# Performance work log

Hardware: AMD Instinct MI355X
Metric: run time of the kernel (lower is better)

## Reference

```python
import jax, jax.numpy as jnp
import numpy as np

DX = 8e-6      # pixel pitch (m)
Z = 0.05       # propagation distance (m)
B, C, H, W = 8, 3, 1024, 1024


def setup_inputs() -> dict:
    key = jax.random.key(0)
    k1, k2 = jax.random.split(key)
    x_real = jax.random.normal(k1, (B, C, H, W), dtype=jnp.float32)
    x_imag = jax.random.normal(k2, (B, C, H, W), dtype=jnp.float32)
    wavelengths = jnp.asarray([450e-9, 532e-9, 632.8e-9], dtype=jnp.float32)
    return {"x_real": x_real, "x_imag": x_imag, "wavelengths": wavelengths}


def _transfer_function(wavelengths, h, w, dx, z):
    # Angular-spectrum transfer function per wavelength: [C, H, W] complex64
    fx = jnp.fft.fftfreq(w, d=dx).astype(jnp.float32)  # [W]
    fy = jnp.fft.fftfreq(h, d=dx).astype(jnp.float32)  # [H]
    f2 = fy[:, None] ** 2 + fx[None, :] ** 2           # [H, W]
    lam = wavelengths[:, None, None]                   # [C, 1, 1]
    arg = 1.0 - (lam ** 2) * f2[None]                  # [C, H, W]
    kz = (2.0 * jnp.pi / lam) * z * jnp.sqrt(jnp.maximum(arg, 0.0))
    Hc = jnp.exp(1j * kz.astype(jnp.complex64))
    # zero out evanescent components
    return jnp.where(arg > 0.0, Hc, jnp.zeros((), dtype=jnp.complex64))


def reference(x_real, x_imag, wavelengths):
    # Batched angular-spectrum propagation, one wavelength per channel.
    x = (x_real + 1j * x_imag).astype(jnp.complex64)   # [B, C, H, W]
    Hc = _transfer_function(wavelengths, H, W, DX, Z)  # [C, H, W]
    Xf = jnp.fft.fft2(x, axes=(-2, -1))
    out = jnp.fft.ifft2(Xf * Hc[None], axes=(-2, -1))  # [B, C, H, W] complex
    # return real/imag stacked so output is a float tensor: [2, B, C, H, W]
    return jnp.stack([out.real.astype(jnp.float32), out.imag.astype(jnp.float32)], axis=0)
```

## Files before the change

kernel.cpp:

```cpp
#include <hip/hip_runtime.h>
#include <math.h>


#define NIMG 24

__device__ __forceinline__ float2 cadd(float2 a, float2 b){ return make_float2(a.x+b.x, a.y+b.y); }
__device__ __forceinline__ float2 csub(float2 a, float2 b){ return make_float2(a.x-b.x, a.y-b.y); }
__device__ __forceinline__ float2 cmul(float2 a, float c, float s){ return make_float2(a.x*c - a.y*s, a.x*s + a.y*c); }

__device__ __forceinline__ int SW(int j) {
    int b = j << 3;
    return b ^ (((b >> 7) & 7) << 4);
}

__device__ __forceinline__ float2 computeH(float lam, int ky, int kx) {
    int iy = (ky < 512) ? ky : ky - 1024;
    int ix = (kx < 512) ? kx : kx - 1024;
    const double recip = 1.0 / (1024.0 * 8e-06);
    float fy = (float)((double)iy * recip);
    float fx = (float)((double)ix * recip);
    float f2  = __fadd_rn(__fmul_rn(fy, fy), __fmul_rn(fx, fx));
    float l2  = __fmul_rn(lam, lam);
    float arg = __fsub_rn(1.0f, __fmul_rn(l2, f2));
    float2 h = make_float2(0.0f, 0.0f);
    if (arg > 0.0f) {
        float t  = __fdiv_rn(6.28318530717958647692f, lam);
        t        = __fmul_rn(t, 0.05f);
        float kz = __fmul_rn(t, __fsqrt_rn(arg));
        double s, c;
        sincos((double)kz, &s, &c);
        const float sc = 9.5367431640625e-07f;
        h = make_float2((float)c * sc, (float)s * sc);
    }
    return h;
}

__global__ __launch_bounds__(256) void build_H_T(float2* __restrict__ Htab,
                                                 const float* __restrict__ wl) {
    int idx = blockIdx.x * 256 + threadIdx.x;
    int c   = idx >> 20;
    int rem = idx & 1048575;
    Htab[idx] = computeH(wl[c], rem & 1023, rem >> 10);
}

template<int SIGN>
__device__ __forceinline__ void dft4nt(float2& a0, float2& a1, float2& a2, float2& a3) {
    float2 t0 = cadd(a0, a2), t1 = csub(a0, a2);
    float2 t2 = cadd(a1, a3), t3 = csub(a1, a3);
    a0 = cadd(t0, t2);
    a2 = csub(t0, t2);
    a1 = make_float2(t1.x - SIGN * t3.y, t1.y + SIGN * t3.x);
    a3 = make_float2(t1.x + SIGN * t3.y, t1.y - SIGN * t3.x);
}
template<int SIGN>
__device__ __forceinline__ void dft4(float2& a0, float2& a1, float2& a2, float2& a3,
                                     float c1, float s1) {
    float c2 = c1*c1 - s1*s1, s2 = 2.f*c1*s1;
    float c3 = c2*c1 - s2*s1, s3 = s2*c1 + c2*s1;
    a1 = cmul(a1, c1, s1);
    a2 = cmul(a2, c2, s2);
    a3 = cmul(a3, c3, s3);
    dft4nt<SIGN>(a0, a1, a2, a3);
}

#define WSYNC() do { asm volatile("s_waitcnt lgkmcnt(0)" ::: "memory"); \
                     __builtin_amdgcn_wave_barrier(); } while (0)


__device__ __forceinline__ void ldsToRegs(char* cb, int l, float2 (&v)[4][4]) {
    const int swzE = (((l >> 4)    ) & 7) << 4;
    const int swzO = (((l >> 4) + 4) & 7) << 4;
    char* rbE = cb + ((8 * l) ^ swzE);
    char* rbO = cb + ((8 * l) ^ swzO);
    #pragma unroll
    for (int k = 0; k < 4; ++k) {
        #pragma unroll
        for (int r = 0; r < 4; ++r) {
            const int tt = k + 4 * r;
            v[k][r] = *(const float2*)(((tt & 1) ? rbO : rbE) + 512 * tt);
        }
    }
}

template<int SIGN>
__device__ __forceinline__ void fftA(char* cb, int l, float2 (&v)[4][4]) {
    const float SPI8 = SIGN * 0.39269908169872415481f;
    #pragma unroll
    for (int k = 0; k < 4; ++k) dft4nt<SIGN>(v[k][0], v[k][1], v[k][2], v[k][3]);
    dft4nt<SIGN>(v[0][0], v[1][0], v[2][0], v[3][0]);
    #pragma unroll
    for (int q = 1; q < 4; ++q) {
        float s1, c1; __sincosf((float)q * SPI8, &s1, &c1);
        dft4<SIGN>(v[0][q], v[1][q], v[2][q], v[3][q], c1, s1);
    }
    char* wb = cb + 128 * l;
    const int L7 = l & 7;
    #pragma unroll
    for (int p = 0; p < 4; ++p) {
        *(float4*)(wb + 16 * ((2*p+0) ^ L7)) =
            make_float4(v[p][0].x, v[p][0].y, v[p][1].x, v[p][1].y);
        *(float4*)(wb + 16 * ((2*p+1) ^ L7)) =
            make_float4(v[p][2].x, v[p][2].y, v[p][3].x, v[p][3].y);
    }
}

template<int SIGN>
__device__ __forceinline__ void fftB(char* cb, int l) {
    const float SPI32  = SIGN * 0.09817477042468103870f;
    const float SPI128 = SIGN * 0.02454369260617025967f;
    const int swzE = (((l >> 4)    ) & 7) << 4;
    const int swzO = (((l >> 4) + 4) & 7) << 4;
    char* rbE = cb + ((8 * l) ^ swzE);
    char* rbO = cb + ((8 * l) ^ swzO);
    float2 v[4][4];
    #pragma unroll
    for (int k = 0; k < 4; ++k) {
        #pragma unroll
        for (int r = 0; r < 4; ++r) {
            const int tt = k + 4 * r;
            v[k][r] = *(const float2*)(((tt & 1) ? rbO : rbE) + 512 * tt);
        }
    }
    const int jm2 = l & 15;
    float s1, c1; __sincosf((float)jm2 * SPI32, &s1, &c1);
    #pragma unroll
    for (int k = 0; k < 4; ++k) dft4<SIGN>(v[k][0], v[k][1], v[k][2], v[k][3], c1, s1);
    const int lo8 = 8 * (l & 15);
    const int hi  = 2048 * (l >> 4);
    #pragma unroll
    for (int q = 0; q < 4; ++q) {
        float s1b, c1b; __sincosf((float)(jm2 + 16 * q) * SPI128, &s1b, &c1b);
        dft4<SIGN>(v[0][q], v[1][q], v[2][q], v[3][q], c1b, s1b);
        #pragma unroll
        for (int p = 0; p < 4; ++p) {
            const int K = ((q + 4 * p) & 7) << 4;
            *(float2*)(cb + (lo8 ^ K) + hi + 128 * q + 512 * p) = v[p][q];
        }
    }
}

template<int SIGN>
__device__ __forceinline__ void fftC(int l, float2 (&v)[4][4]) {
    const float SPI512 = SIGN * 0.00613592315154256492f;
    #pragma unroll
    for (int m = 0; m < 4; ++m) {
        float s1, c1; __sincosf((float)(l + 64 * m) * SPI512, &s1, &c1);
        dft4<SIGN>(v[m][0], v[m][1], v[m][2], v[m][3], c1, s1);
    }
}

__global__ __launch_bounds__(1024) void k1_rows_T16(const float* __restrict__ xr,
                                                    const float* __restrict__ xi,
                                                    float2* __restrict__ T) {
    extern __shared__ char lds[];
    const int t = threadIdx.x, w = t >> 6, l = t & 63;
    const int img = blockIdx.x >> 6;
    const int b0  = blockIdx.x & 63;
    const int y0  = b0 << 4;
    const long long ib = (long long)img << 20;
    char* cb = lds + 8192 * w;

    const float* rr = xr + ib + (long long)(y0 + w) * 1024;
    const float* ri = xi + ib + (long long)(y0 + w) * 1024;
    float2 v[4][4];
    #pragma unroll
    for (int k = 0; k < 4; ++k) {
        #pragma unroll
        for (int r = 0; r < 4; ++r) {
            const int p = l + 64 * (k + 4 * r);
            v[k][r] = make_float2(rr[p], ri[p]);
        }
    }
    fftA<-1>(cb, l, v); WSYNC();
    fftB<-1>(cb, l);    WSYNC();
    ldsToRegs(cb, l, v);
    fftC<-1>(l, v);
    __syncthreads();

    {
        const int w8 = w << 3;
        #pragma unroll
        for (int m = 0; m < 4; ++m) {
            #pragma unroll
            for (int q = 0; q < 4; ++q) {
                const int p  = l + 64 * (m + 4 * q);
                const int sx = (((p >> 1) & 7) << 4) | (((p >> 4) & 1) << 3);
                *(float2*)(lds + p * 128 + (w8 ^ sx)) = v[m][q];
            }
        }
    }
    __syncthreads();

    {
        const int j = l >> 3;
        const int xbase = (w << 3) + (l & 7);
        const bool sw = (w >> 1) & 1;
        #pragma unroll
        for (int i = 0; i < 8; ++i) {
            const int x   = xbase + (i << 7);
            const int s70 = ((x >> 1) & 7) << 4;
            float4 g = *(const float4*)(lds + x * 128 + ((16 * j) ^ s70));
            if (sw) g = make_float4(g.z, g.w, g.x, g.y);
            const int rb = (b0 + x) & 63;
            *(float4*)(T + ib + (long long)x * 1024 + (rb << 4) + 2 * j) = g;
        }
    }
}

__global__ __launch_bounds__(256, 4) void k2_cols_H(float2* __restrict__ T,
                                                    const float2* __restrict__ Htab,
                                                    const float* __restrict__ wl) {
    __shared__ float4 ldsb[2048];
    char* lds = (char*)ldsb;
    const int t = threadIdx.x, w = t >> 6, l = t & 63;
    const int img = blockIdx.x >> 8;
    const int x   = ((blockIdx.x & 255) << 2) + w;
    const int lamIdx = img % 3;
    char* cb = lds + 8192 * w;
    float2* col = T + ((long long)img << 20) + (long long)x * 1024;

    const int xl15 = l & 15, lhi = l >> 4;
    #define CIDX(tt) (((((lhi) + 4 * (tt) + x) & 63) << 4) + xl15)

    float2 v[4][4];
    #pragma unroll
    for (int k = 0; k < 4; ++k) {
        #pragma unroll
        for (int r = 0; r < 4; ++r)
            v[k][r] = col[CIDX(k + 4 * r)];
    }
    fftA<-1>(cb, l, v); WSYNC();
    fftB<-1>(cb, l);    WSYNC();

    float2 h[4][4];
    if (Htab) {
        const float2* hrow = Htab + ((long long)lamIdx << 20) + (long long)x * 1024;
        #pragma unroll
        for (int m = 0; m < 4; ++m) {
            #pragma unroll
            for (int q = 0; q < 4; ++q)
                h[m][q] = hrow[l + 64 * (m + 4 * q)];
        }
    } else {
        const float lam = wl[lamIdx];
        #pragma unroll
        for (int m = 0; m < 4; ++m) {
            #pragma unroll
            for (int q = 0; q < 4; ++q)
                h[m][q] = computeH(lam, l + 64 * (m + 4 * q), x);
        }
    }

    ldsToRegs(cb, l, v);
    fftC<-1>(l, v);

    #pragma unroll
    for (int m = 0; m < 4; ++m) {
        #pragma unroll
        for (int q = 0; q < 4; ++q) {
            float2 a = v[m][q], hh = h[m][q];
            v[m][q] = make_float2(a.x * hh.x - a.y * hh.y, a.x * hh.y + a.y * hh.x);
        }
    }
    WSYNC();

    fftA<1>(cb, l, v); WSYNC();
    fftB<1>(cb, l);    WSYNC();
    ldsToRegs(cb, l, v);
    fftC<1>(l, v);

    #pragma unroll
    for (int m = 0; m < 4; ++m) {
        #pragma unroll
        for (int q = 0; q < 4; ++q)
            col[CIDX(m + 4 * q)] = v[m][q];
    }
    #undef CIDX
}

__global__ __launch_bounds__(1024) void k3_irows_T16(const float2* __restrict__ T,
                                                     float* __restrict__ outr,
                                                     float* __restrict__ outi) {
    extern __shared__ char lds[];
    const int t = threadIdx.x, w = t >> 6, l = t & 63;
    const int img = blockIdx.x >> 6;
    const int b0  = blockIdx.x & 63;
    const int y0  = b0 << 4;
    const long long ib = (long long)img << 20;

    {
        const int rb = (b0 + t) & 63;
        const float4* src = (const float4*)(T + ib + (long long)t * 1024 + (rb << 4));
        const int sx = SW(t);
        #pragma unroll
        for (int p = 0; p < 8; ++p) {
            float4 g = src[p];
            *(float2*)(lds + 8192 * (2 * p)     + sx) = make_float2(g.x, g.y);
            *(float2*)(lds + 8192 * (2 * p + 1) + sx) = make_float2(g.z, g.w);
        }
    }
    __syncthreads();

    char* cb = lds + 8192 * w;
    float2 v[4][4];
    ldsToRegs(cb, l, v);
    fftA<1>(cb, l, v); WSYNC();
    fftB<1>(cb, l);    WSYNC();
    ldsToRegs(cb, l, v);
    fftC<1>(l, v);

    float* pr = outr + ib + (long long)(y0 + w) * 1024;
    float* pi = outi + ib + (long long)(y0 + w) * 1024;
    #pragma unroll
    for (int m = 0; m < 4; ++m) {
        #pragma unroll
        for (int q = 0; q < 4; ++q) {
            const int p = l + 64 * (m + 4 * q);
            pr[p] = v[m][q].x;
            pi[p] = v[m][q].y;
        }
    }
}

extern "C" void kernel_launch(void* const* d_in, const int* in_sizes, int n_in,
                              void* d_out, int out_size, void* d_ws, size_t ws_size,
                              hipStream_t stream) {
    const float* xr = (const float*)d_in[0];
    const float* xi = (const float*)d_in[1];
    const float* wl = (const float*)d_in[2];
    float* out = (float*)d_out;

    const size_t planeElems = (size_t)NIMG * 1024 * 1024;
    float2* wsC = (float2*)d_ws;
    const size_t needC = planeElems * sizeof(float2);
    const size_t needH = (size_t)3 * 1024 * 1024 * sizeof(float2);
    float2* Htab = nullptr;
    if (ws_size >= needC + needH) {
        Htab = (float2*)((char*)d_ws + needC);
        build_H_T<<<12288, 256, 0, stream>>>(Htab, wl);
    }
    k1_rows_T16<<<NIMG * 64, 1024, 131072, stream>>>(xr, xi, wsC);
    k2_cols_H<<<NIMG * 256, 256, 0, stream>>>(wsC, Htab, wl);
    k3_irows_T16<<<NIMG * 64, 1024, 131072, stream>>>(wsC, out, out + planeElems);
}
```

Baseline: 350.2 us.

## Store intermediate spectrum in row-block tiled layout with contiguous per-block writes

```diff
diff --git a/kernel.cpp b/kernel.cpp
--- a/kernel.cpp
+++ b/kernel.cpp
@@ -7,11 +7,6 @@
 __device__ __forceinline__ float2 cadd(float2 a, float2 b){ return make_float2(a.x+b.x, a.y+b.y); }
 __device__ __forceinline__ float2 csub(float2 a, float2 b){ return make_float2(a.x-b.x, a.y-b.y); }
 __device__ __forceinline__ float2 cmul(float2 a, float c, float s){ return make_float2(a.x*c - a.y*s, a.x*s + a.y*c); }
-
-__device__ __forceinline__ int SW(int j) {
-    int b = j << 3;
-    return b ^ (((b >> 7) & 7) << 4);
-}
 
 __device__ __forceinline__ float2 computeH(float lam, int ky, int kx) {
     int iy = (ky < 512) ? ky : ky - 1024;
@@ -149,9 +144,10 @@
     }
 }
 
-__global__ __launch_bounds__(1024) void k1_rows_T16(const float* __restrict__ xr,
-                                                    const float* __restrict__ xi,
-                                                    float2* __restrict__ T) {
+
+__global__ __launch_bounds__(1024) void k1_rows_A(const float* __restrict__ xr,
+                                                  const float* __restrict__ xi,
+                                                  float2* __restrict__ A) {
     extern __shared__ char lds[];
     const int t = threadIdx.x, w = t >> 6, l = t & 63;
     const int img = blockIdx.x >> 6;
@@ -192,42 +188,39 @@
     __syncthreads();
 
     {
-        const int j = l >> 3;
-        const int xbase = (w << 3) + (l & 7);
-        const bool sw = (w >> 1) & 1;
+        float4* dst = (float4*)(A + ib + (long long)b0 * 16384);
         #pragma unroll
         for (int i = 0; i < 8; ++i) {
-            const int x   = xbase + (i << 7);
+            const int fidx = t + 1024 * i;
+            const int x  = fidx >> 3, yj = fidx & 7;
             const int s70 = ((x >> 1) & 7) << 4;
-            float4 g = *(const float4*)(lds + x * 128 + ((16 * j) ^ s70));
-            if (sw) g = make_float4(g.z, g.w, g.x, g.y);
-            const int rb = (b0 + x) & 63;
-            *(float4*)(T + ib + (long long)x * 1024 + (rb << 4) + 2 * j) = g;
-        }
-    }
-}
-
-__global__ __launch_bounds__(256, 4) void k2_cols_H(float2* __restrict__ T,
+            float4 g = *(const float4*)(lds + x * 128 + ((16 * yj) ^ s70));
+            if ((x >> 4) & 1) g = make_float4(g.z, g.w, g.x, g.y);
+            dst[fidx] = g;
+        }
+    }
+}
+
+__global__ __launch_bounds__(512, 4) void k2_cols_H(float2* __restrict__ A,
                                                     const float2* __restrict__ Htab,
                                                     const float* __restrict__ wl) {
-    __shared__ float4 ldsb[2048];
+    __shared__ float4 ldsb[4096];
     char* lds = (char*)ldsb;
     const int t = threadIdx.x, w = t >> 6, l = t & 63;
-    const int img = blockIdx.x >> 8;
-    const int x   = ((blockIdx.x & 255) << 2) + w;
+    const int img = (NIMG - 1) - (blockIdx.x >> 7);
+    const int x   = ((blockIdx.x & 127) << 3) + w;
     const int lamIdx = img % 3;
     char* cb = lds + 8192 * w;
-    float2* col = T + ((long long)img << 20) + (long long)x * 1024;
-
-    const int xl15 = l & 15, lhi = l >> 4;
-    #define CIDX(tt) (((((lhi) + 4 * (tt) + x) & 63) << 4) + xl15)
+
+    float2* colA = A + ((long long)img << 20) + x * 16 + (l & 15);
+    const int bl = (l >> 4) << 14;
 
     float2 v[4][4];
     #pragma unroll
     for (int k = 0; k < 4; ++k) {
         #pragma unroll
         for (int r = 0; r < 4; ++r)
-            v[k][r] = col[CIDX(k + 4 * r)];
+            v[k][r] = colA[bl + (k + 4 * r) * 65536];
     }
     fftA<-1>(cb, l, v); WSYNC();
     fftB<-1>(cb, l);    WSYNC();
@@ -273,14 +266,13 @@
     for (int m = 0; m < 4; ++m) {
         #pragma unroll
         for (int q = 0; q < 4; ++q)
-            col[CIDX(m + 4 * q)] = v[m][q];
-    }
-    #undef CIDX
-}
-
-__global__ __launch_bounds__(1024) void k3_irows_T16(const float2* __restrict__ T,
-                                                     float* __restrict__ outr,
-                                                     float* __restrict__ outi) {
+            colA[bl + (m + 4 * q) * 65536] = v[m][q];
+    }
+}
+
+__global__ __launch_bounds__(1024) void k3_irows_A(const float2* __restrict__ A,
+                                                   float* __restrict__ outr,
+                                                   float* __restrict__ outi) {
     extern __shared__ char lds[];
     const int t = threadIdx.x, w = t >> 6, l = t & 63;
     const int img = blockIdx.x >> 6;
@@ -289,21 +281,35 @@
     const long long ib = (long long)img << 20;
 
     {
-        const int rb = (b0 + t) & 63;
-        const float4* src = (const float4*)(T + ib + (long long)t * 1024 + (rb << 4));
-        const int sx = SW(t);
-        #pragma unroll
-        for (int p = 0; p < 8; ++p) {
-            float4 g = src[p];
-            *(float2*)(lds + 8192 * (2 * p)     + sx) = make_float2(g.x, g.y);
-            *(float2*)(lds + 8192 * (2 * p + 1) + sx) = make_float2(g.z, g.w);
+        const float4* src = (const float4*)(A + ib + (long long)b0 * 16384);
+        #pragma unroll
+        for (int i = 0; i < 8; ++i) {
+            const int fidx = t + 1024 * i;
+            const int x  = fidx >> 3, yj = fidx & 7;
+            const int s70 = ((x >> 1) & 7) << 4;
+            float4 g = src[fidx];
+            if ((x >> 4) & 1) g = make_float4(g.z, g.w, g.x, g.y);
+            *(float4*)(lds + x * 128 + ((16 * yj) ^ s70)) = g;
         }
     }
     __syncthreads();
 
+    float2 v[4][4];
+    {
+        const int w8 = w << 3;
+        #pragma unroll
+        for (int m = 0; m < 4; ++m) {
+            #pragma unroll
+            for (int q = 0; q < 4; ++q) {
+                const int p  = l + 64 * (m + 4 * q);
+                const int sx = (((p >> 1) & 7) << 4) | (((p >> 4) & 1) << 3);
+                v[m][q] = *(const float2*)(lds + p * 128 + (w8 ^ sx));
+            }
+        }
+    }
+    __syncthreads();
+
     char* cb = lds + 8192 * w;
-    float2 v[4][4];
-    ldsToRegs(cb, l, v);
     fftA<1>(cb, l, v); WSYNC();
     fftB<1>(cb, l);    WSYNC();
     ldsToRegs(cb, l, v);
@@ -331,15 +337,15 @@
     float* out = (float*)d_out;
 
     const size_t planeElems = (size_t)NIMG * 1024 * 1024;
-    float2* wsC = (float2*)d_ws;
-    const size_t needC = planeElems * sizeof(float2);
+    float2* A = (float2*)d_ws;
+    const size_t needA = planeElems * sizeof(float2);
     const size_t needH = (size_t)3 * 1024 * 1024 * sizeof(float2);
     float2* Htab = nullptr;
-    if (ws_size >= needC + needH) {
-        Htab = (float2*)((char*)d_ws + needC);
+    if (ws_size >= needA + needH) {
+        Htab = (float2*)((char*)d_ws + needA);
         build_H_T<<<12288, 256, 0, stream>>>(Htab, wl);
     }
-    k1_rows_T16<<<NIMG * 64, 1024, 131072, stream>>>(xr, xi, wsC);
-    k2_cols_H<<<NIMG * 256, 256, 0, stream>>>(wsC, Htab, wl);
-    k3_irows_T16<<<NIMG * 64, 1024, 131072, stream>>>(wsC, out, out + planeElems);
-}
+    k1_rows_A<<<NIMG * 64, 1024, 131072, stream>>>(xr, xi, A);
+    k2_cols_H<<<NIMG * 128, 512, 0, stream>>>(A, Htab, wl);
+    k3_irows_A<<<NIMG * 64, 1024, 131072, stream>>>(A, out, out + planeElems);
+}
```

Result: faster. 334.4 us (-4.5%).
